# Kernel tuning notes

Hardware: AMD Instinct MI355X
Metric: run time of the kernel (lower is better)

Reference implementation:

```python
import jax, jax.numpy as jnp
import numpy as np

B, S, H, C = 128, 2048, 1024, 256
N_LANGS = 8


def setup_inputs() -> dict:
    key = jax.random.key(0)
    ks = jax.random.split(key, 7)
    features = jax.random.normal(ks[0], (B, S, H), dtype=jnp.float32)
    language_ids = jax.random.randint(ks[1], (B,), 0, N_LANGS, dtype=jnp.int64)
    attention_mask = jnp.ones((B, S), dtype=jnp.int32)
    # projection MLP params (stored as [in, out]; math-equivalent to torch Linear)
    W1 = jax.random.normal(ks[2], (H, H), dtype=jnp.float32) / np.sqrt(H)
    b1 = jnp.zeros((H,), dtype=jnp.float32)
    W2 = jax.random.normal(ks[3], (H, C), dtype=jnp.float32) / np.sqrt(H)
    b2 = jnp.zeros((C,), dtype=jnp.float32)
    temperature = jnp.array([0.07], dtype=jnp.float32)
    return {"features": features, "W1": W1, "b1": b1, "W2": W2, "b2": b2,
            "temperature": temperature, "language_ids": language_ids,
            "attention_mask": attention_mask}


def reference(features, W1, b1, W2, b2, temperature, language_ids, attention_mask):
    # masked mean pool over seq: [B,S,H] -> [B,H]
    m = attention_mask.astype(features.dtype)[:, :, None]
    pooled = (features * m).sum(axis=1) / m.sum(axis=1)
    # MLP projection head
    h = jax.nn.relu(pooled @ W1 + b1)
    proj = h @ W2 + b2
    # L2 normalize (torch F.normalize eps=1e-12)
    norm = jnp.maximum(jnp.linalg.norm(proj, axis=-1, keepdims=True), 1e-12)
    proj = proj / norm
    # similarity matrix [B,B]
    sim = (proj @ proj.T) / temperature[0]
    # vectorized replacement of the O(B^2) python label loop
    b = language_ids.shape[0]
    diff_lang = language_ids[:, None] != language_ids[None, :]
    off_diag = ~jnp.eye(b, dtype=bool)
    labels = (diff_lang & off_diag).astype(sim.dtype)
    # torch F.cross_entropy with soft (probability) targets:
    # mean over rows of -sum_j labels[i,j] * log_softmax(sim)[i,j]
    logp = jax.nn.log_softmax(sim, axis=-1)
    loss = jnp.mean(-(labels * logp).sum(axis=-1))
    return proj, loss
```

## Files before the change

kernel.cpp:

```cpp
#include <hip/hip_runtime.h>
#include <math.h>

#define BATCH 128
#define SEQ   2048
#define HID   1024
#define CDIM  256
#define SPLIT 16
#define ROWS_PER (SEQ / SPLIT)
#define KC1   16

typedef float vf4 __attribute__((ext_vector_type(4)));
typedef int   vi4 __attribute__((ext_vector_type(4)));

__global__ __launch_bounds__(256) void pool_partial_kernel(
    const float* __restrict__ feat, const int* __restrict__ mask,
    float* __restrict__ partial, int* __restrict__ cntp,
    unsigned* __restrict__ counter)
{
    const int b     = blockIdx.x;
    const int chunk = blockIdx.y;
    const int t     = threadIdx.x;

    const vf4* fp = reinterpret_cast<const vf4*>(feat) +
                    ((size_t)b * SEQ + (size_t)chunk * ROWS_PER) * (HID / 4);
    const vi4* mp = reinterpret_cast<const vi4*>(
                        mask + (size_t)b * SEQ + (size_t)chunk * ROWS_PER);

    vf4 acc = {0.f, 0.f, 0.f, 0.f};
    int csum = 0;
    for (int s = 0; s < ROWS_PER; s += 8) {
        const vi4 m0 = mp[s / 4];
        const vi4 m1 = mp[s / 4 + 1];
        csum += m0.x + m0.y + m0.z + m0.w + m1.x + m1.y + m1.z + m1.w;
        float mm[8];
        mm[0] = (float)m0.x; mm[1] = (float)m0.y; mm[2] = (float)m0.z; mm[3] = (float)m0.w;
        mm[4] = (float)m1.x; mm[5] = (float)m1.y; mm[6] = (float)m1.z; mm[7] = (float)m1.w;
        #pragma unroll
        for (int u = 0; u < 8; ++u) {
            const vf4 v = __builtin_nontemporal_load(&fp[(size_t)(s + u) * (HID / 4) + t]);
            acc += v * mm[u];
        }
    }
    reinterpret_cast<vf4*>(partial)[((size_t)b * SPLIT + chunk) * (HID / 4) + t] = acc;
    if (t == 0) {
        cntp[b * SPLIT + chunk] = csum;
        if (b == 0 && chunk == 0) *counter = 0u;
    }
}

__global__ __launch_bounds__(256) void mlp1_fused_kernel(
    const float* __restrict__ partial, const int* __restrict__ cntp,
    const float* __restrict__ W1, float* __restrict__ part1)
{
    const int jc = blockIdx.x;
    const int bg = blockIdx.y;
    const int kc = blockIdx.z;
    const int t  = threadIdx.x;

    __shared__ float ps[8][64];
    __shared__ float invs[8];

    if (t < 8) {
        const int* cp = cntp + (size_t)(bg * 8 + t) * SPLIT;
        int c = 0;
        #pragma unroll
        for (int p = 0; p < SPLIT; ++p) c += cp[p];
        invs[t] = 1.0f / (float)c;
    }

    const int r  = t >> 4;
    const int c4 = t & 15;
    vf4 acc4 = {0.f, 0.f, 0.f, 0.f};
    if (t < 128) {
        const vf4* pp = reinterpret_cast<const vf4*>(partial);
        #pragma unroll
        for (int p = 0; p < SPLIT; ++p)
            acc4 += pp[((size_t)(bg * 8 + r) * SPLIT + p) * (HID / 4) + kc * 16 + c4];
    }
    __syncthreads();
    if (t < 128)
        *reinterpret_cast<vf4*>(&ps[r][c4 * 4]) = acc4 * invs[r];
    __syncthreads();

    const int j = jc * 256 + t;
    const float* w = W1 + (size_t)(kc * 64) * HID + j;

    float acc[8];
    #pragma unroll
    for (int rr = 0; rr < 8; ++rr) acc[rr] = 0.f;

    #pragma unroll
    for (int k = 0; k < 64; k += 8) {
        float wv[8];
        #pragma unroll
        for (int u = 0; u < 8; ++u) wv[u] = w[(size_t)(k + u) * HID];
        #pragma unroll
        for (int u = 0; u < 8; ++u) {
            #pragma unroll
            for (int rr = 0; rr < 8; ++rr)
                acc[rr] = fmaf(ps[rr][k + u], wv[u], acc[rr]);
        }
    }
    #pragma unroll
    for (int rr = 0; rr < 8; ++rr)
        part1[((size_t)kc * BATCH + bg * 8 + rr) * HID + j] = acc[rr];
}

__global__ __launch_bounds__(1024) void mlp2_full_kernel(
    const float* __restrict__ part1, const float* __restrict__ b1,
    const float* __restrict__ W2, const float* __restrict__ b2,
    float* __restrict__ proj)
{
    const int b  = blockIdx.x;
    const int t  = threadIdx.x;
    const int j  = t & 255;
    const int kc = t >> 8;

    __shared__ float hs[HID];
    __shared__ float pacc[4][CDIM];
    __shared__ float red[CDIM];

    float s = b1[t];
    #pragma unroll
    for (int p = 0; p < KC1; ++p)
        s += part1[((size_t)p * BATCH + b) * HID + t];
    hs[t] = fmaxf(s, 0.f);
    __syncthreads();

    const float* w = W2 + (size_t)(kc * 256) * CDIM + j;
    const float* h = hs + kc * 256;
    float acc = 0.f;
    #pragma unroll
    for (int k = 0; k < 256; k += 8) {
        float wv[8];
        #pragma unroll
        for (int u = 0; u < 8; ++u) wv[u] = w[(size_t)(k + u) * CDIM];
        #pragma unroll
        for (int u = 0; u < 8; ++u) acc = fmaf(h[k + u], wv[u], acc);
    }
    pacc[kc][j] = acc;
    __syncthreads();

    float tot = 0.f;
    if (t < CDIM) {
        tot = b2[t] + pacc[0][t] + pacc[1][t] + pacc[2][t] + pacc[3][t];
        red[t] = tot * tot;
    }
    __syncthreads();
    for (int off = CDIM / 2; off > 0; off >>= 1) {
        if (t < off) red[t] += red[t + off];
        __syncthreads();
    }
    if (t < CDIM) {
        const float norm = fmaxf(sqrtf(red[0]), 1e-12f);
        proj[(size_t)b * CDIM + t] = tot / norm;
    }
}

__global__ __launch_bounds__(128) void sim_loss_kernel(
    const float* __restrict__ proj, const float* __restrict__ temp,
    const int* __restrict__ lang, float* __restrict__ loss_part,
    unsigned* __restrict__ counter, float* __restrict__ out_loss)
{
    const int i = blockIdx.x;
    const int j = threadIdx.x;

    __shared__ float pi[CDIM];
    if (j < CDIM / 4)
        reinterpret_cast<vf4*>(pi)[j] =
            reinterpret_cast<const vf4*>(proj + (size_t)i * CDIM)[j];
    __syncthreads();

    const vf4* pj = reinterpret_cast<const vf4*>(proj + (size_t)j * CDIM);
    float acc = 0.f;
    #pragma unroll 8
    for (int c = 0; c < CDIM / 4; ++c) {
        const vf4 v = pj[c];
        acc = fmaf(pi[4 * c + 0], v.x, acc);
        acc = fmaf(pi[4 * c + 1], v.y, acc);
        acc = fmaf(pi[4 * c + 2], v.z, acc);
        acc = fmaf(pi[4 * c + 3], v.w, acc);
    }
    const float s = acc / temp[0];
    const int li = lang[i];

    __shared__ float r1[BATCH];
    __shared__ int   ci[BATCH];

    r1[j] = s;
    __syncthreads();
    for (int off = BATCH / 2; off > 0; off >>= 1) {
        if (j < off) r1[j] = fmaxf(r1[j], r1[j + off]);
        __syncthreads();
    }
    const float m = r1[0];
    __syncthreads();

    r1[j] = expf(s - m);
    __syncthreads();
    for (int off = BATCH / 2; off > 0; off >>= 1) {
        if (j < off) r1[j] += r1[j + off];
        __syncthreads();
    }
    const float lse = m + logf(r1[0]);
    __syncthreads();

    const bool sel = (lang[j] != li) && (j != i);
    r1[j] = sel ? s : 0.f;
    ci[j] = sel ? 1 : 0;
    __syncthreads();
    for (int off = BATCH / 2; off > 0; off >>= 1) {
        if (j < off) { r1[j] += r1[j + off]; ci[j] += ci[j + off]; }
        __syncthreads();
    }

    __shared__ bool last;
    if (j == 0) {
        loss_part[i] = (float)ci[0] * lse - r1[0];
        __threadfence();
        const unsigned old = atomicAdd(counter, 1u);
        last = (old == BATCH - 1);
    }
    __syncthreads();
    if (last) {
        __threadfence();
        r1[j] = loss_part[j];
        __syncthreads();
        for (int off = BATCH / 2; off > 0; off >>= 1) {
            if (j < off) r1[j] += r1[j + off];
            __syncthreads();
        }
        if (j == 0) out_loss[0] = r1[0] / (float)BATCH;
    }
}

extern "C" void kernel_launch(void* const* d_in, const int* in_sizes, int n_in,
                              void* d_out, int out_size, void* d_ws, size_t ws_size,
                              hipStream_t stream)
{
    const float* feat = (const float*)d_in[0];
    const float* W1   = (const float*)d_in[1];
    const float* b1   = (const float*)d_in[2];
    const float* W2   = (const float*)d_in[3];
    const float* b2   = (const float*)d_in[4];
    const float* temp = (const float*)d_in[5];
    const int*   lang = (const int*)d_in[6];
    const int*   amask= (const int*)d_in[7];
    float* out = (float*)d_out;
    float* ws  = (float*)d_ws;

    float*    partial   = ws;
    float*    part1     = partial + (size_t)BATCH * SPLIT * HID;
    float*    loss_part = part1 + (size_t)KC1 * BATCH * HID;
    int*      cntp      = (int*)(loss_part + BATCH);
    unsigned* counter   = (unsigned*)(cntp + BATCH * SPLIT);

    pool_partial_kernel<<<dim3(BATCH, SPLIT), 256, 0, stream>>>(
        feat, amask, partial, cntp, counter);
    mlp1_fused_kernel<<<dim3(HID / 256, BATCH / 8, KC1), 256, 0, stream>>>(
        partial, cntp, W1, part1);
    mlp2_full_kernel<<<BATCH, 1024, 0, stream>>>(part1, b1, W2, b2, out);
    sim_loss_kernel<<<BATCH, BATCH, 0, stream>>>(
        out, temp, lang, loss_part, counter, out + (size_t)BATCH * CDIM);
}
```

Baseline: 210.5 us.

## Reduce pooled partials and MLP2 splits in last-arriving blocks via atomic tickets

The pooling kernel now uses a per-batch atomic ticket so the last chunk block sums the SPLIT partials and writes the final pooled vector once. MLP1 then reads pooled rows directly instead of re-reducing the partials in every block. MLP2 is split across 4 blocks per batch row, up from one 1024-thread block, and the last block adds the partials and normalizes. Tickets are cleared with a memset launch, which adds an extra stream operation plus threadfence/atomic overhead in exchange for less redundant partial reading and more blocks in MLP2.

```diff
diff --git a/kernel.cpp b/kernel.cpp
--- a/kernel.cpp
+++ b/kernel.cpp
@@ -8,14 +8,15 @@
 #define SPLIT 16
 #define ROWS_PER (SEQ / SPLIT)
 #define KC1   16
+#define KC2   4
 
 typedef float vf4 __attribute__((ext_vector_type(4)));
 typedef int   vi4 __attribute__((ext_vector_type(4)));
 
-__global__ __launch_bounds__(256) void pool_partial_kernel(
+__global__ __launch_bounds__(256) void pool_fused_kernel(
     const float* __restrict__ feat, const int* __restrict__ mask,
     float* __restrict__ partial, int* __restrict__ cntp,
-    unsigned* __restrict__ counter)
+    unsigned* __restrict__ ticket, float* __restrict__ pooled)
 {
     const int b     = blockIdx.x;
     const int chunk = blockIdx.y;
@@ -42,15 +43,32 @@
         }
     }
     reinterpret_cast<vf4*>(partial)[((size_t)b * SPLIT + chunk) * (HID / 4) + t] = acc;
-    if (t == 0) {
-        cntp[b * SPLIT + chunk] = csum;
-        if (b == 0 && chunk == 0) *counter = 0u;
-    }
-}
-
-__global__ __launch_bounds__(256) void mlp1_fused_kernel(
-    const float* __restrict__ partial, const int* __restrict__ cntp,
-    const float* __restrict__ W1, float* __restrict__ part1)
+    if (t == 0) cntp[b * SPLIT + chunk] = csum;
+
+    __shared__ unsigned oldv;
+    __threadfence();
+    if (t == 0) oldv = atomicAdd(&ticket[b], 1u);
+    __syncthreads();
+    if (oldv == SPLIT - 1) {
+        __threadfence();
+        int c = 0;
+        #pragma unroll
+        for (int p = 0; p < SPLIT; ++p) c += cntp[b * SPLIT + p];
+        const float inv = 1.0f / (float)c;
+
+        const vf4* pp = reinterpret_cast<const vf4*>(partial);
+        vf4 a = {0.f, 0.f, 0.f, 0.f};
+        #pragma unroll
+        for (int p = 0; p < SPLIT; ++p)
+            a += pp[((size_t)b * SPLIT + p) * (HID / 4) + t];
+        a *= inv;
+        reinterpret_cast<vf4*>(pooled)[(size_t)b * (HID / 4) + t] = a;
+    }
+}
+
+__global__ __launch_bounds__(256) void mlp1_partial_kernel(
+    const float* __restrict__ pooled, const float* __restrict__ W1,
+    float* __restrict__ part1)
 {
     const int jc = blockIdx.x;
     const int bg = blockIdx.y;
@@ -58,28 +76,12 @@
     const int t  = threadIdx.x;
 
     __shared__ float ps[8][64];
-    __shared__ float invs[8];
-
-    if (t < 8) {
-        const int* cp = cntp + (size_t)(bg * 8 + t) * SPLIT;
-        int c = 0;
-        #pragma unroll
-        for (int p = 0; p < SPLIT; ++p) c += cp[p];
-        invs[t] = 1.0f / (float)c;
-    }
-
-    const int r  = t >> 4;
-    const int c4 = t & 15;
-    vf4 acc4 = {0.f, 0.f, 0.f, 0.f};
     if (t < 128) {
-        const vf4* pp = reinterpret_cast<const vf4*>(partial);
-        #pragma unroll
-        for (int p = 0; p < SPLIT; ++p)
-            acc4 += pp[((size_t)(bg * 8 + r) * SPLIT + p) * (HID / 4) + kc * 16 + c4];
-    }
-    __syncthreads();
-    if (t < 128)
-        *reinterpret_cast<vf4*>(&ps[r][c4 * 4]) = acc4 * invs[r];
+        const int r = t >> 4;
+        const int c = (t & 15) * 4;
+        *reinterpret_cast<vf4*>(&ps[r][c]) =
+            *reinterpret_cast<const vf4*>(&pooled[(size_t)(bg * 8 + r) * HID + kc * 64 + c]);
+    }
     __syncthreads();
 
     const int j = jc * 256 + t;
@@ -87,7 +89,7 @@
 
     float acc[8];
     #pragma unroll
-    for (int rr = 0; rr < 8; ++rr) acc[rr] = 0.f;
+    for (int r = 0; r < 8; ++r) acc[r] = 0.f;
 
     #pragma unroll
     for (int k = 0; k < 64; k += 8) {
@@ -97,38 +99,34 @@
         #pragma unroll
         for (int u = 0; u < 8; ++u) {
             #pragma unroll
-            for (int rr = 0; rr < 8; ++rr)
-                acc[rr] = fmaf(ps[rr][k + u], wv[u], acc[rr]);
-        }
-    }
-    #pragma unroll
-    for (int rr = 0; rr < 8; ++rr)
-        part1[((size_t)kc * BATCH + bg * 8 + rr) * HID + j] = acc[rr];
-}
-
-__global__ __launch_bounds__(1024) void mlp2_full_kernel(
+            for (int r = 0; r < 8; ++r)
+                acc[r] = fmaf(ps[r][k + u], wv[u], acc[r]);
+        }
+    }
+    #pragma unroll
+    for (int r = 0; r < 8; ++r)
+        part1[((size_t)kc * BATCH + bg * 8 + r) * HID + j] = acc[r];
+}
+
+__global__ __launch_bounds__(256) void mlp2_fused_kernel(
     const float* __restrict__ part1, const float* __restrict__ b1,
     const float* __restrict__ W2, const float* __restrict__ b2,
+    float* __restrict__ part2, unsigned* __restrict__ ticket,
     float* __restrict__ proj)
 {
     const int b  = blockIdx.x;
+    const int kc = blockIdx.y;
     const int t  = threadIdx.x;
-    const int j  = t & 255;
-    const int kc = t >> 8;
-
-    __shared__ float hs[HID];
-    __shared__ float pacc[4][CDIM];
-    __shared__ float red[CDIM];
-
-    float s = b1[t];
+
+    __shared__ float hs[256];
+    float s = b1[kc * 256 + t];
     #pragma unroll
     for (int p = 0; p < KC1; ++p)
-        s += part1[((size_t)p * BATCH + b) * HID + t];
+        s += part1[((size_t)p * BATCH + b) * HID + kc * 256 + t];
     hs[t] = fmaxf(s, 0.f);
     __syncthreads();
 
-    const float* w = W2 + (size_t)(kc * 256) * CDIM + j;
-    const float* h = hs + kc * 256;
+    const float* w = W2 + (size_t)(kc * 256) * CDIM + t;
     float acc = 0.f;
     #pragma unroll
     for (int k = 0; k < 256; k += 8) {
@@ -136,22 +134,28 @@
         #pragma unroll
         for (int u = 0; u < 8; ++u) wv[u] = w[(size_t)(k + u) * CDIM];
         #pragma unroll
-        for (int u = 0; u < 8; ++u) acc = fmaf(h[k + u], wv[u], acc);
-    }
-    pacc[kc][j] = acc;
-    __syncthreads();
-
-    float tot = 0.f;
-    if (t < CDIM) {
-        tot = b2[t] + pacc[0][t] + pacc[1][t] + pacc[2][t] + pacc[3][t];
+        for (int u = 0; u < 8; ++u) acc = fmaf(hs[k + u], wv[u], acc);
+    }
+    part2[((size_t)kc * BATCH + b) * CDIM + t] = acc;
+
+    __shared__ unsigned oldv;
+    __threadfence();
+    if (t == 0) oldv = atomicAdd(&ticket[b], 1u);
+    __syncthreads();
+    if (oldv == KC2 - 1) {
+        __threadfence();
+        float tot = b2[t];
+        #pragma unroll
+        for (int p = 0; p < KC2; ++p)
+            tot += part2[((size_t)p * BATCH + b) * CDIM + t];
+
+        __shared__ float red[CDIM];
         red[t] = tot * tot;
-    }
-    __syncthreads();
-    for (int off = CDIM / 2; off > 0; off >>= 1) {
-        if (t < off) red[t] += red[t + off];
-        __syncthreads();
-    }
-    if (t < CDIM) {
+        __syncthreads();
+        for (int off = CDIM / 2; off > 0; off >>= 1) {
+            if (t < off) red[t] += red[t + off];
+            __syncthreads();
+        }
         const float norm = fmaxf(sqrtf(red[0]), 1e-12f);
         proj[(size_t)b * CDIM + t] = tot / norm;
     }
@@ -250,16 +254,25 @@
     float* ws  = (float*)d_ws;
 
     float*    partial   = ws;
-    float*    part1     = partial + (size_t)BATCH * SPLIT * HID;
-    float*    loss_part = part1 + (size_t)KC1 * BATCH * HID;
+    float*    pooled    = partial + (size_t)BATCH * SPLIT * HID;
+    float*    part1     = pooled + (size_t)BATCH * HID;
+    float*    part2     = part1 + (size_t)KC1 * BATCH * HID;
+    float*    loss_part = part2 + (size_t)KC2 * BATCH * CDIM;
     int*      cntp      = (int*)(loss_part + BATCH);
-    unsigned* counter   = (unsigned*)(cntp + BATCH * SPLIT);
-
-    pool_partial_kernel<<<dim3(BATCH, SPLIT), 256, 0, stream>>>(
-        feat, amask, partial, cntp, counter);
-    mlp1_fused_kernel<<<dim3(HID / 256, BATCH / 8, KC1), 256, 0, stream>>>(
-        partial, cntp, W1, part1);
-    mlp2_full_kernel<<<BATCH, 1024, 0, stream>>>(part1, b1, W2, b2, out);
+    unsigned* tickets   = (unsigned*)(cntp + BATCH * SPLIT);
+
+    hipMemsetAsync(tickets, 0, (2 * BATCH + 1) * sizeof(unsigned), stream);
+
+    unsigned* tkt_pool = tickets;
+    unsigned* tkt_mlp2 = tickets + BATCH;
+    unsigned* tkt_loss = tickets + 2 * BATCH;
+
+    pool_fused_kernel<<<dim3(BATCH, SPLIT), 256, 0, stream>>>(
+        feat, amask, partial, cntp, tkt_pool, pooled);
+    mlp1_partial_kernel<<<dim3(HID / 256, BATCH / 8, KC1), 256, 0, stream>>>(
+        pooled, W1, part1);
+    mlp2_fused_kernel<<<dim3(BATCH, KC2), 256, 0, stream>>>(
+        part1, b1, W2, b2, part2, tkt_mlp2, out);
     sim_loss_kernel<<<BATCH, BATCH, 0, stream>>>(
-        out, temp, lang, loss_part, counter, out + (size_t)BATCH * CDIM);
-}
+        out, temp, lang, loss_part, tkt_loss, out + (size_t)BATCH * CDIM);
+}
```

New measurement: 723.8 us. 3.44x slower.

## Split MLP2 across k-chunks into partial+final kernels and parallelize pooled reduction

Applied to the files above, without the earlier changes.

The single 1024-thread-per-batch MLP2 kernel becomes a partial kernel over a (batch, k-chunk) grid of 256-thread blocks, followed by a separate kernel that adds bias, reduces the chunks and L2-normalizes. In the MLP1 kernel, all 256 threads now reduce the split-pool partials (two halves of 8 each) instead of only 128 threads. The aim is better occupancy and more parallelism in the small reduction stages. The cost is an extra kernel launch and a workspace round trip for the MLP2 partials.

```diff
diff --git a/kernel.cpp b/kernel.cpp
--- a/kernel.cpp
+++ b/kernel.cpp
@@ -8,6 +8,7 @@
 #define SPLIT 16
 #define ROWS_PER (SEQ / SPLIT)
 #define KC1   16
+#define KC2   4
 
 typedef float vf4 __attribute__((ext_vector_type(4)));
 typedef int   vi4 __attribute__((ext_vector_type(4)));
@@ -15,7 +16,7 @@
 __global__ __launch_bounds__(256) void pool_partial_kernel(
     const float* __restrict__ feat, const int* __restrict__ mask,
     float* __restrict__ partial, int* __restrict__ cntp,
-    unsigned* __restrict__ counter)
+    unsigned* __restrict__ tkt_loss)
 {
     const int b     = blockIdx.x;
     const int chunk = blockIdx.y;
@@ -44,7 +45,7 @@
     reinterpret_cast<vf4*>(partial)[((size_t)b * SPLIT + chunk) * (HID / 4) + t] = acc;
     if (t == 0) {
         cntp[b * SPLIT + chunk] = csum;
-        if (b == 0 && chunk == 0) *counter = 0u;
+        if (b == 0 && chunk == 0) *tkt_loss = 0u;
     }
 }
 
@@ -57,8 +58,22 @@
     const int kc = blockIdx.z;
     const int t  = threadIdx.x;
 
-    __shared__ float ps[8][64];
+    __shared__ float psA[8][64];
+    __shared__ float psB[8][64];
     __shared__ float invs[8];
+
+    const int half = t >> 7;
+    const int idx  = t & 127;
+    const int r    = idx >> 4;
+    const int c4   = idx & 15;
+
+    const vf4* pp = reinterpret_cast<const vf4*>(partial);
+    const size_t base = ((size_t)(bg * 8 + r) * SPLIT + half * 8) * (HID / 4)
+                        + (size_t)kc * 16 + c4;
+    vf4 a = {0.f, 0.f, 0.f, 0.f};
+    #pragma unroll
+    for (int p = 0; p < 8; ++p)
+        a += pp[base + (size_t)p * (HID / 4)];
 
     if (t < 8) {
         const int* cp = cntp + (size_t)(bg * 8 + t) * SPLIT;
@@ -68,18 +83,15 @@
         invs[t] = 1.0f / (float)c;
     }
 
-    const int r  = t >> 4;
-    const int c4 = t & 15;
-    vf4 acc4 = {0.f, 0.f, 0.f, 0.f};
-    if (t < 128) {
-        const vf4* pp = reinterpret_cast<const vf4*>(partial);
-        #pragma unroll
-        for (int p = 0; p < SPLIT; ++p)
-            acc4 += pp[((size_t)(bg * 8 + r) * SPLIT + p) * (HID / 4) + kc * 16 + c4];
-    }
-    __syncthreads();
-    if (t < 128)
-        *reinterpret_cast<vf4*>(&ps[r][c4 * 4]) = acc4 * invs[r];
+    float* dst = half ? &psB[0][0] : &psA[0][0];
+    *reinterpret_cast<vf4*>(dst + r * 64 + c4 * 4) = a;
+    __syncthreads();
+
+    if (half == 0) {
+        vf4 s = (*reinterpret_cast<vf4*>(&psA[r][c4 * 4]) +
+                 *reinterpret_cast<vf4*>(&psB[r][c4 * 4])) * invs[r];
+        *reinterpret_cast<vf4*>(&psA[r][c4 * 4]) = s;
+    }
     __syncthreads();
 
     const int j = jc * 256 + t;
@@ -98,7 +110,7 @@
         for (int u = 0; u < 8; ++u) {
             #pragma unroll
             for (int rr = 0; rr < 8; ++rr)
-                acc[rr] = fmaf(ps[rr][k + u], wv[u], acc[rr]);
+                acc[rr] = fmaf(psA[rr][k + u], wv[u], acc[rr]);
         }
     }
     #pragma unroll
@@ -106,29 +118,23 @@
         part1[((size_t)kc * BATCH + bg * 8 + rr) * HID + j] = acc[rr];
 }
 
-__global__ __launch_bounds__(1024) void mlp2_full_kernel(
+__global__ __launch_bounds__(256) void mlp2_partial_kernel(
     const float* __restrict__ part1, const float* __restrict__ b1,
-    const float* __restrict__ W2, const float* __restrict__ b2,
-    float* __restrict__ proj)
+    const float* __restrict__ W2, float* __restrict__ part2)
 {
     const int b  = blockIdx.x;
+    const int kc = blockIdx.y;
     const int t  = threadIdx.x;
-    const int j  = t & 255;
-    const int kc = t >> 8;
-
-    __shared__ float hs[HID];
-    __shared__ float pacc[4][CDIM];
-    __shared__ float red[CDIM];
-
-    float s = b1[t];
+
+    __shared__ float hs[256];
+    float s = b1[kc * 256 + t];
     #pragma unroll
     for (int p = 0; p < KC1; ++p)
-        s += part1[((size_t)p * BATCH + b) * HID + t];
+        s += part1[((size_t)p * BATCH + b) * HID + kc * 256 + t];
     hs[t] = fmaxf(s, 0.f);
     __syncthreads();
 
-    const float* w = W2 + (size_t)(kc * 256) * CDIM + j;
-    const float* h = hs + kc * 256;
+    const float* w = W2 + (size_t)(kc * 256) * CDIM + t;
     float acc = 0.f;
     #pragma unroll
     for (int k = 0; k < 256; k += 8) {
@@ -136,25 +142,32 @@
         #pragma unroll
         for (int u = 0; u < 8; ++u) wv[u] = w[(size_t)(k + u) * CDIM];
         #pragma unroll
-        for (int u = 0; u < 8; ++u) acc = fmaf(h[k + u], wv[u], acc);
-    }
-    pacc[kc][j] = acc;
-    __syncthreads();
-
-    float tot = 0.f;
-    if (t < CDIM) {
-        tot = b2[t] + pacc[0][t] + pacc[1][t] + pacc[2][t] + pacc[3][t];
-        red[t] = tot * tot;
-    }
+        for (int u = 0; u < 8; ++u) acc = fmaf(hs[k + u], wv[u], acc);
+    }
+    part2[((size_t)kc * BATCH + b) * CDIM + t] = acc;
+}
+
+__global__ __launch_bounds__(256) void mlp2_final_kernel(
+    const float* __restrict__ part2, const float* __restrict__ b2,
+    float* __restrict__ proj)
+{
+    const int b = blockIdx.x;
+    const int t = threadIdx.x;
+
+    float acc = b2[t];
+    #pragma unroll
+    for (int p = 0; p < KC2; ++p)
+        acc += part2[((size_t)p * BATCH + b) * CDIM + t];
+
+    __shared__ float red[CDIM];
+    red[t] = acc * acc;
     __syncthreads();
     for (int off = CDIM / 2; off > 0; off >>= 1) {
         if (t < off) red[t] += red[t + off];
         __syncthreads();
     }
-    if (t < CDIM) {
-        const float norm = fmaxf(sqrtf(red[0]), 1e-12f);
-        proj[(size_t)b * CDIM + t] = tot / norm;
-    }
+    const float norm = fmaxf(sqrtf(red[0]), 1e-12f);
+    proj[(size_t)b * CDIM + t] = acc / norm;
 }
 
 __global__ __launch_bounds__(128) void sim_loss_kernel(
@@ -251,15 +264,18 @@
 
     float*    partial   = ws;
     float*    part1     = partial + (size_t)BATCH * SPLIT * HID;
-    float*    loss_part = part1 + (size_t)KC1 * BATCH * HID;
+    float*    part2     = part1 + (size_t)KC1 * BATCH * HID;
+    float*    loss_part = part2 + (size_t)KC2 * BATCH * CDIM;
     int*      cntp      = (int*)(loss_part + BATCH);
-    unsigned* counter   = (unsigned*)(cntp + BATCH * SPLIT);
+    unsigned* tkt_loss  = (unsigned*)(cntp + BATCH * SPLIT);
 
     pool_partial_kernel<<<dim3(BATCH, SPLIT), 256, 0, stream>>>(
-        feat, amask, partial, cntp, counter);
+        feat, amask, partial, cntp, tkt_loss);
     mlp1_fused_kernel<<<dim3(HID / 256, BATCH / 8, KC1), 256, 0, stream>>>(
         partial, cntp, W1, part1);
-    mlp2_full_kernel<<<BATCH, 1024, 0, stream>>>(part1, b1, W2, b2, out);
+    mlp2_partial_kernel<<<dim3(BATCH, KC2), 256, 0, stream>>>(
+        part1, b1, W2, part2);
+    mlp2_final_kernel<<<BATCH, CDIM, 0, stream>>>(part2, b2, out);
     sim_loss_kernel<<<BATCH, BATCH, 0, stream>>>(
-        out, temp, lang, loss_part, counter, out + (size_t)BATCH * CDIM);
-}
+        out, temp, lang, loss_part, tkt_loss, out + (size_t)BATCH * CDIM);
+}
```

Result: no change. 208.4 us (-1.0%).
